# Performance work log

Measured on AMD Instinct MI355X. Metric: run time of the kernel, lower is better.

## Reference

```python
import jax, jax.numpy as jnp
import numpy as np

N_CLUSTERS = 16
D_SUB = 256          # d = n_z / n_clusters
ETA = 5.0
TEMPERATURE = 0.1
EPS = 1e-08


def _l2_normalize(x, axis):
    # matches torch F.normalize(p=2, eps=1e-8): x / max(||x||, eps)
    norm = jnp.sqrt(jnp.sum(x * x, axis=axis, keepdims=True))
    return x / jnp.maximum(norm, EPS)


def setup_inputs() -> dict:
    key = jax.random.key(0)
    k1, k2 = jax.random.split(key)
    z = jax.random.normal(k1, (16384, 4096), dtype=jnp.float32)
    D = jax.random.normal(k2, (4096, 4096), dtype=jnp.float32)
    return {"z": z, "D": D}


def reference(z, D):
    # Per-cluster loop in the original: normalize each column-slice D_i along
    # dim 0, mm, square-sum. Column-wise normalization of each slice equals
    # column-wise normalization of the whole D, so fuse into one GEMM.
    z_norm = _l2_normalize(z, axis=1)            # [N, n_z]
    D_norm = _l2_normalize(D, axis=0)            # [n_z, n_z]
    sim = z_norm @ D_norm                        # [N, n_z]
    N = sim.shape[0]
    # sum of squared similarities within each cluster's d columns
    s = jnp.sum(jnp.square(sim).reshape(N, N_CLUSTERS, D_SUB), axis=2)  # [N, K]
    s = s / TEMPERATURE + ETA * D_SUB
    s = jax.nn.softmax(s, axis=1)
    return (s, z)
```

## Files before the change

kernel.cpp:

```cpp
#include <hip/hip_runtime.h>

#define M_DIM 16384
#define N_DIM 4096
#define K_DIM 4096
#define NCLUST 16

#define BM 256
#define BN 128
#define KB4 2048
#define TKB 64
#define NT 32

typedef unsigned short u16;
typedef unsigned char u8;
typedef float floatx4 __attribute__((ext_vector_type(4)));
typedef int int4v __attribute__((ext_vector_type(4)));
typedef int int8v __attribute__((ext_vector_type(8)));

typedef const unsigned int __attribute__((address_space(1))) gu32;
typedef unsigned int __attribute__((address_space(3))) lu32;

__device__ __forceinline__ unsigned f2fp4(float x) {
  unsigned s = (__float_as_uint(x) >> 28) & 0x8u;
  float ax = fabsf(x);
  unsigned m;
  if      (ax < 0.25f) m = 0;
  else if (ax < 0.75f) m = 1;
  else if (ax < 1.25f) m = 2;
  else if (ax < 1.75f) m = 3;
  else if (ax < 2.5f)  m = 4;
  else if (ax < 3.5f)  m = 5;
  else if (ax < 5.0f)  m = 6;
  else                 m = 7;
  return s | m;
}

__global__ __launch_bounds__(256) void zero_kernel(float* __restrict__ p, int n) {
  int i = blockIdx.x * 256 + threadIdx.x;
  if (i < n) p[i] = 0.f;
}

__global__ __launch_bounds__(256) void znorm_kernel(const float* __restrict__ z,
                                                    u8* __restrict__ zn) {
  const int row = blockIdx.x;
  const int t = threadIdx.x;
  const size_t base = (size_t)row * K_DIM;
  const float4* zr = (const float4*)(z + base);
  float4 v[4];
  float ss = 0.f;
#pragma unroll
  for (int i = 0; i < 4; i++) {
    v[i] = zr[t * 4 + i];
    ss += v[i].x * v[i].x + v[i].y * v[i].y + v[i].z * v[i].z + v[i].w * v[i].w;
  }
#pragma unroll
  for (int m = 1; m <= 32; m <<= 1) ss += __shfl_xor(ss, m, 64);
  __shared__ float red[4];
  if ((t & 63) == 0) red[t >> 6] = ss;
  __syncthreads();
  float tot = red[0] + red[1] + red[2] + red[3];
  float sc = 64.0f / fmaxf(sqrtf(tot), 1e-8f);
  uint2* znr = (uint2*)(zn + (size_t)row * KB4);
  unsigned wlo = 0, whi = 0;
#pragma unroll
  for (int i = 0; i < 4; i++) {
    unsigned p = f2fp4(v[i].x * sc) | (f2fp4(v[i].y * sc) << 4) |
                 (f2fp4(v[i].z * sc) << 8) | (f2fp4(v[i].w * sc) << 12);
    if (i < 2) wlo |= p << (16 * i); else whi |= p << (16 * (i - 2));
  }
  uint2 pk; pk.x = wlo; pk.y = whi;
  znr[t] = pk;
}

__global__ __launch_bounds__(256) void colsq_kernel(const float* __restrict__ D,
                                                    float* __restrict__ colsq) {
  const int col = blockIdx.x * 256 + threadIdx.x;
  const int r0 = blockIdx.y * 128;
  float ss = 0.f;
#pragma unroll 4
  for (int r = 0; r < 128; r++) {
    float d = D[(size_t)(r0 + r) * N_DIM + col];
    ss += d * d;
  }
  atomicAdd(&colsq[col], ss);
}

__global__ __launch_bounds__(256) void dnt_kernel(const float* __restrict__ D,
                                                  const float* __restrict__ colsq,
                                                  u8* __restrict__ dnt) {
  __shared__ float tile[64][65];
  const int c0 = blockIdx.x * 64, r0 = blockIdx.y * 64;
  const int t = threadIdx.x;
  const int tr = t >> 4;
  const int tc = (t & 15) * 4;
#pragma unroll
  for (int i = 0; i < 4; i++) {
    int row = i * 16 + tr;
    float4 v = *(const float4*)(D + (size_t)(r0 + row) * N_DIM + c0 + tc);
    tile[row][tc + 0] = v.x; tile[row][tc + 1] = v.y;
    tile[row][tc + 2] = v.z; tile[row][tc + 3] = v.w;
  }
  __syncthreads();
#pragma unroll
  for (int i = 0; i < 4; i++) {
    int nl = i * 16 + tr;
    float sc = 64.0f / fmaxf(sqrtf(colsq[c0 + nl]), 1e-8f);
    u16 pk = (u16)(f2fp4(tile[tc + 0][nl] * sc) | (f2fp4(tile[tc + 1][nl] * sc) << 4) |
                   (f2fp4(tile[tc + 2][nl] * sc) << 8) | (f2fp4(tile[tc + 3][nl] * sc) << 12));
    *(u16*)(dnt + (size_t)(c0 + nl) * KB4 + ((r0 + tc) >> 1)) = pk;
  }
}

__global__ __launch_bounds__(512, 1) void gemm_kernel(const u8* __restrict__ zn,
                                                      const u8* __restrict__ dnt,
                                                      const float* __restrict__ zsrc,
                                                      float* __restrict__ out1,
                                                      float* __restrict__ s_part) {
  __shared__ u8 ldsA[3 * BM * TKB];
  __shared__ u8 ldsB[3 * BN * TKB];

  const int t = threadIdx.x;
  const int w = t >> 6, l = t & 63;
  const int lr = l & 15, lk = l >> 4;

  const int bid = blockIdx.x;
  const int swz = (bid & 7) * 256 + (bid >> 3);
  const int bx = swz & 31, by = swz >> 5;
  const int bm = by * BM, bn = bx * BN;
  const int wm = (w >> 1) * 64, wn = (w & 1) * 64;

  const int sslot = (t & 3) ^ ((t >> 3) & 3);
  const u8* pA = zn + (size_t)(bm + (t >> 2)) * KB4 + sslot * 16;
  const u8* pB = dnt + (size_t)(bn + (t >> 2)) * KB4 + sslot * 16;

#define STAGE(OA, KT) do { \
    __builtin_amdgcn_global_load_lds((gu32*)(pA + (KT) * TKB), \
        (lu32*)&ldsA[(OA) + w * 1024], 16, 0, 0); \
    __builtin_amdgcn_global_load_lds((gu32*)(pA + (size_t)128 * KB4 + (KT) * TKB), \
        (lu32*)&ldsA[(OA) + 8192 + w * 1024], 16, 0, 0); \
    __builtin_amdgcn_global_load_lds((gu32*)(pB + (KT) * TKB), \
        (lu32*)&ldsB[((OA) >> 1) + w * 1024], 16, 0, 0); \
  } while (0)

  int aOff[4], bOff[4];
#pragma unroll
  for (int m = 0; m < 4; m++) {
    int row = wm + m * 16 + lr;
    aOff[m] = row * TKB + ((lk ^ ((row >> 1) & 3)) * 16);
  }
#pragma unroll
  for (int n = 0; n < 4; n++) {
    int row = wn + n * 16 + lr;
    bOff[n] = row * TKB + ((lk ^ ((row >> 1) & 3)) * 16);
  }

  int8v af[4], bf[4];
  floatx4 acc[4][4] = {};

#define LDFRAG(F, base, off) do { \
    int4v* _h = (int4v*)&(F); \
    _h[0] = *(const int4v*)((base) + (off)); \
    _h[1] = (int4v){0, 0, 0, 0}; \
  } while (0)

#define READ_ALL(OA) do { \
    const u8* _ab = ldsA + (OA); \
    const u8* _bb = ldsB + ((OA) >> 1); \
    _Pragma("unroll") \
    for (int ni = 0; ni < 4; ni++) LDFRAG(bf[ni], _bb, bOff[ni]); \
    _Pragma("unroll") \
    for (int mi = 0; mi < 4; mi++) LDFRAG(af[mi], _ab, aOff[mi]); \
  } while (0)

#define MFMA_H(M0) do { \
    __builtin_amdgcn_s_setprio(1); \
    _Pragma("unroll") \
    for (int mi = 0; mi < 2; mi++) \
      _Pragma("unroll") \
      for (int ni = 0; ni < 4; ni++) \
        acc[(M0) + mi][ni] = __builtin_amdgcn_mfma_scale_f32_16x16x128_f8f6f4( \
            af[(M0) + mi], bf[ni], acc[(M0) + mi][ni], 4, 4, 0, 127u, 0, 127u); \
    __builtin_amdgcn_s_setprio(0); \
  } while (0)

#define VM3 asm volatile("s_waitcnt vmcnt(3)" ::: "memory")
#define VM0 asm volatile("s_waitcnt vmcnt(0)" ::: "memory")

#define ITER(OC, ON, STG, WT, RDNEXT) do { \
    __builtin_amdgcn_s_barrier(); \
    __builtin_amdgcn_sched_barrier(0); \
    STG; \
    MFMA_H(0); \
    WT; \
    if (RDNEXT) { \
      LDFRAG(af[0], ldsA + (ON), aOff[0]); \
      LDFRAG(af[1], ldsA + (ON), aOff[1]); \
    } \
    MFMA_H(2); \
    if (RDNEXT) { \
      const u8* _bb = ldsB + ((ON) >> 1); \
      _Pragma("unroll") \
      for (int ni = 0; ni < 4; ni++) LDFRAG(bf[ni], _bb, bOff[ni]); \
      LDFRAG(af[2], ldsA + (ON), aOff[2]); \
      LDFRAG(af[3], ldsA + (ON), aOff[3]); \
    } \
  } while (0)

#define O0 0
#define O1 16384
#define O2 32768

  STAGE(O0, 0); STAGE(O1, 1);
  VM3;
  __builtin_amdgcn_s_barrier();
  READ_ALL(O0);

  for (int kt = 0; kt < NT - 2; kt += 3) {
    ITER(O0, O1, STAGE(O2, kt + 2), VM3, 1);
    ITER(O1, O2, STAGE(O0, kt + 3), VM3, 1);
    ITER(O2, O0, STAGE(O1, kt + 4), VM3, 1);
  }
  ITER(O0, O1, ((void)0), VM0, 1);
  ITER(O1, O1, ((void)0), ((void)0), 0);

#undef ITER
#undef READ_ALL
#undef O0
#undef O1
#undef O2
#undef VM3
#undef VM0
#undef MFMA_H
#undef LDFRAG
#undef STAGE

  __syncthreads();
  float* red = (float*)ldsA;
#pragma unroll
  for (int m = 0; m < 4; m++) {
#pragma unroll
    for (int r = 0; r < 4; r++) {
      float v = 0.f;
#pragma unroll
      for (int n = 0; n < 4; n++) { float x = acc[m][n][r]; v += x * x; }
      v += __shfl_xor(v, 1, 64);
      v += __shfl_xor(v, 2, 64);
      v += __shfl_xor(v, 4, 64);
      v += __shfl_xor(v, 8, 64);
      if (lr == 0) {
        int lrow = wm + m * 16 + lk * 4 + r;
        red[lrow * 2 + (w & 1)] = v;
      }
    }
  }
  __syncthreads();
  if (t < 256) {
    float s = red[t * 2 + 0] + red[t * 2 + 1];
    s_part[((size_t)(bm + t) * NCLUST + (bx >> 1)) * 2 + (bx & 1)] = s;
  }

  {
    const float4* cs = (const float4*)zsrc + (size_t)bid * 8192 + t;
    float4* cd = (float4*)out1 + (size_t)bid * 8192 + t;
#pragma unroll
    for (int j = 0; j < 16; j += 4) {
      float4 a0 = cs[(j + 0) * 512];
      float4 a1 = cs[(j + 1) * 512];
      float4 a2 = cs[(j + 2) * 512];
      float4 a3 = cs[(j + 3) * 512];
      cd[(j + 0) * 512] = a0;
      cd[(j + 1) * 512] = a1;
      cd[(j + 2) * 512] = a2;
      cd[(j + 3) * 512] = a3;
    }
  }
}

__global__ __launch_bounds__(256) void softmax_kernel(const float* __restrict__ s_part,
                                                      float* __restrict__ out0) {
  int r = blockIdx.x * 256 + threadIdx.x;
  const float4* sp = (const float4*)(s_part + (size_t)r * 32);
  float v[16];
#pragma unroll
  for (int i = 0; i < 8; i++) {
    float4 a = sp[i];
    v[i * 2 + 0] = a.x + a.y;
    v[i * 2 + 1] = a.z + a.w;
  }
  const float lsc = 5.9604644775390625e-7f;
  float mx = -1e30f;
#pragma unroll
  for (int i = 0; i < 16; i++) { v[i] *= lsc; mx = fmaxf(mx, v[i]); }
  float sum = 0.f;
#pragma unroll
  for (int i = 0; i < 16; i++) { v[i] = __expf(v[i] - mx); sum += v[i]; }
  float rs = 1.0f / sum;
  float4* op = (float4*)(out0 + (size_t)r * 16);
#pragma unroll
  for (int i = 0; i < 4; i++) {
    float4 a;
    a.x = v[i * 4 + 0] * rs; a.y = v[i * 4 + 1] * rs;
    a.z = v[i * 4 + 2] * rs; a.w = v[i * 4 + 3] * rs;
    op[i] = a;
  }
}

extern "C" void kernel_launch(void* const* d_in, const int* in_sizes, int n_in,
                              void* d_out, int out_size, void* d_ws, size_t ws_size,
                              hipStream_t stream) {
  const float* z = (const float*)d_in[0];
  const float* D = (const float*)d_in[1];
  float* out0 = (float*)d_out;
  float* out1 = out0 + (size_t)M_DIM * NCLUST;

  char* ws = (char*)d_ws;
  u8* zn   = (u8*)ws;
  u8* dnt  = (u8*)(ws + (size_t)M_DIM * KB4);
  float* colsq  = (float*)(ws + (size_t)M_DIM * KB4 + (size_t)N_DIM * KB4);
  float* s_part = colsq + N_DIM;

  zero_kernel<<<(N_DIM + 255) / 256, 256, 0, stream>>>(colsq, N_DIM);
  znorm_kernel<<<M_DIM, 256, 0, stream>>>(z, zn);
  colsq_kernel<<<dim3(N_DIM / 256, N_DIM / 128), 256, 0, stream>>>(D, colsq);
  dnt_kernel<<<dim3(N_DIM / 64, N_DIM / 64), 256, 0, stream>>>(D, colsq, dnt);
  gemm_kernel<<<(M_DIM / BM) * (N_DIM / BN), 512, 0, stream>>>(zn, dnt, z, out1, s_part);
  softmax_kernel<<<M_DIM / 256, 256, 0, stream>>>(s_part, out0);
}
```

Baseline: 386.3 us.

## Interleave z passthrough copy into GEMM main loop instead of epilogue

The per-block copy of z into the second output moves out of the serial epilogue. Each main-loop iteration now stores one float2 chunk and prefetches the next, so the copy traffic overlaps with the MFMA work. The vmcnt wait rises from 3 to 5 to account for the extra in-flight load and store. The risks are added memory traffic contending with operand staging, and compiler-inserted waits on the copy register stalling the pipeline.

Measured after the change: 419.4 us. 1.09x slower.

```diff
diff --git a/kernel.cpp b/kernel.cpp
--- a/kernel.cpp
+++ b/kernel.cpp
@@ -129,6 +129,10 @@
   const int bm = by * BM, bn = bx * BN;
   const int wm = (w >> 1) * 64, wn = (w & 1) * 64;
 
+  const float2* csrc2 = (const float2*)zsrc + (size_t)bid * 16384 + t;
+  float2* cdst2 = (float2*)out1 + (size_t)bid * 16384 + t;
+  float2 cbuf;
+
   const int sslot = (t & 3) ^ ((t >> 3) & 3);
   const u8* pA = zn + (size_t)(bm + (t >> 2)) * KB4 + sslot * 16;
   const u8* pB = dnt + (size_t)(bn + (t >> 2)) * KB4 + sslot * 16;
@@ -183,13 +187,34 @@
     __builtin_amdgcn_s_setprio(0); \
   } while (0)
 
+#define VM5 asm volatile("s_waitcnt vmcnt(5)" ::: "memory")
 #define VM3 asm volatile("s_waitcnt vmcnt(3)" ::: "memory")
 #define VM0 asm volatile("s_waitcnt vmcnt(0)" ::: "memory")
 
-#define ITER(OC, ON, STG, WT, RDNEXT) do { \
+#define ITER_C(OC, ON, KT2) do { \
     __builtin_amdgcn_s_barrier(); \
     __builtin_amdgcn_sched_barrier(0); \
-    STG; \
+    cdst2[0] = cbuf; \
+    cbuf = csrc2[512]; \
+    csrc2 += 512; cdst2 += 512; \
+    STAGE(KT2##_O, KT2); \
+    MFMA_H(0); \
+    VM5; \
+    LDFRAG(af[0], ldsA + (ON), aOff[0]); \
+    LDFRAG(af[1], ldsA + (ON), aOff[1]); \
+    MFMA_H(2); \
+    { \
+      const u8* _bb = ldsB + ((ON) >> 1); \
+      _Pragma("unroll") \
+      for (int ni = 0; ni < 4; ni++) LDFRAG(bf[ni], _bb, bOff[ni]); \
+      LDFRAG(af[2], ldsA + (ON), aOff[2]); \
+      LDFRAG(af[3], ldsA + (ON), aOff[3]); \
+    } \
+  } while (0)
+
+#define ITER_T(ON, WT, RDNEXT) do { \
+    __builtin_amdgcn_s_barrier(); \
+    __builtin_amdgcn_sched_barrier(0); \
     MFMA_H(0); \
     WT; \
     if (RDNEXT) { \
@@ -210,29 +235,42 @@
 #define O1 16384
 #define O2 32768
 
+  cbuf = csrc2[0];
   STAGE(O0, 0); STAGE(O1, 1);
   VM3;
   __builtin_amdgcn_s_barrier();
   READ_ALL(O0);
 
   for (int kt = 0; kt < NT - 2; kt += 3) {
-    ITER(O0, O1, STAGE(O2, kt + 2), VM3, 1);
-    ITER(O1, O2, STAGE(O0, kt + 3), VM3, 1);
-    ITER(O2, O0, STAGE(O1, kt + 4), VM3, 1);
-  }
-  ITER(O0, O1, ((void)0), VM0, 1);
-  ITER(O1, O1, ((void)0), ((void)0), 0);
-
-#undef ITER
+#define kp2_O O2
+#define kp3_O O0
+#define kp4_O O1
+    { const int kp2 = kt + 2; ITER_C(O0, O1, kp2); }
+    { const int kp3 = kt + 3; ITER_C(O1, O2, kp3); }
+    { const int kp4 = kt + 4; ITER_C(O2, O0, kp4); }
+#undef kp2_O
+#undef kp3_O
+#undef kp4_O
+  }
+  ITER_T(O1, VM0, 1);
+  ITER_T(O1, ((void)0), 0);
+
+#undef ITER_C
+#undef ITER_T
 #undef READ_ALL
 #undef O0
 #undef O1
 #undef O2
+#undef VM5
 #undef VM3
 #undef VM0
 #undef MFMA_H
 #undef LDFRAG
 #undef STAGE
+
+  cdst2[0] = cbuf;
+  float2 clast = csrc2[512];
+  cdst2[512] = clast;
 
   __syncthreads();
   float* red = (float*)ldsA;
@@ -258,22 +296,6 @@
     float s = red[t * 2 + 0] + red[t * 2 + 1];
     s_part[((size_t)(bm + t) * NCLUST + (bx >> 1)) * 2 + (bx & 1)] = s;
   }
-
-  {
-    const float4* cs = (const float4*)zsrc + (size_t)bid * 8192 + t;
-    float4* cd = (float4*)out1 + (size_t)bid * 8192 + t;
-#pragma unroll
-    for (int j = 0; j < 16; j += 4) {
-      float4 a0 = cs[(j + 0) * 512];
-      float4 a1 = cs[(j + 1) * 512];
-      float4 a2 = cs[(j + 2) * 512];
-      float4 a3 = cs[(j + 3) * 512];
-      cd[(j + 0) * 512] = a0;
-      cd[(j + 1) * 512] = a1;
-      cd[(j + 2) * 512] = a2;
-      cd[(j + 3) * 512] = a3;
-    }
-  }
 }
 
 __global__ __launch_bounds__(256) void softmax_kernel(const float* __restrict__ s_part,
```
